# Kernel tuning notes

Measured on AMD Instinct MI355X. Metric: run time of the kernel, lower is better.

Reference implementation:

```python
import jax, jax.numpy as jnp
import numpy as np

B, S, D, H, DH = 2, 2048, 768, 12, 64
ROT, BASE, WIN = 64, 10000.0, 128
SCALE = float(np.sqrt(DH))  # cfg.attn_scale = sqrt(d_head) = 8.0


def _sin_cos():
    # TransformerLens calculate_sin_cos_rotary, rotary_adjacent_pairs=False
    pos = jnp.arange(S, dtype=jnp.float32)
    freq = BASE ** (jnp.arange(0, ROT, 2, dtype=jnp.float32) / ROT)
    freq = jnp.concatenate([freq, freq])  # 'd -> (2 d)'
    angles = pos[:, None] / freq[None, :]  # [S, ROT]
    return jnp.sin(angles), jnp.cos(angles)


def _rotate_every_two(v):
    n = v.shape[-1] // 2
    return jnp.concatenate([-v[..., n:], v[..., :n]], axis=-1)


def _apply_rotary(x, sin, cos):
    # x: [B, S, H, DH]; rotate first ROT dims, pass rest through
    xr, xp = x[..., :ROT], x[..., ROT:]
    c = cos[None, :, None, :]
    s = sin[None, :, None, :]
    return jnp.concatenate([xr * c + _rotate_every_two(xr) * s, xp], axis=-1)


def setup_inputs() -> dict:
    key = jax.random.key(0)
    ks = jax.random.split(key, 7)
    init = lambda k, shape: jax.random.normal(k, shape, jnp.float32) / np.sqrt(D).astype(np.float32)
    return dict(
        query_input=jax.random.normal(ks[0], (B, S, D), jnp.float32),
        key_input=jax.random.normal(ks[1], (B, S, D), jnp.float32),
        value_input=jax.random.normal(ks[2], (B, S, D), jnp.float32),
        W_Q=init(ks[3], (H, D, DH)),
        W_K=init(ks[4], (H, D, DH)),
        W_V=init(ks[5], (H, D, DH)),
        W_O=init(ks[6], (H, DH, D)),
        b_Q=jnp.zeros((H, DH), jnp.float32),
        b_K=jnp.zeros((H, DH), jnp.float32),
        b_V=jnp.zeros((H, DH), jnp.float32),
        b_O=jnp.zeros((D,), jnp.float32),
    )


def reference(query_input, key_input, value_input, W_Q, W_K, W_V, W_O, b_Q, b_K, b_V, b_O):
    # QKV projections (calculate_qkv_matrices)
    q = jnp.einsum('bpd,hdk->bphk', query_input, W_Q) + b_Q
    k = jnp.einsum('bpd,hdk->bphk', key_input, W_K) + b_K
    v = jnp.einsum('bpd,hdk->bphk', value_input, W_V) + b_V
    # rotary (kv_cache_pos_offset = 0)
    sin, cos = _sin_cos()
    q = _apply_rotary(q, sin, cos)
    k = _apply_rotary(k, sin, cos)
    # attention scores
    scores = jnp.einsum('bqhd,bkhd->bhqk', q, k) / SCALE
    # position_bias defaults to zeros -> no-op
    i = jnp.arange(S)[:, None]
    j = jnp.arange(S)[None, :]
    mask = (j <= i) & (j > i - WIN)
    scores = jnp.where(mask[None, None], scores, -jnp.inf)
    pattern = jax.nn.softmax(scores, axis=-1)
    pattern = jnp.where(jnp.isnan(pattern), 0.0, pattern)
    z = jnp.einsum('bhqk,bkhd->bqhd', pattern, v)  # [B, S, H, DH]
    # output projection: z flattened @ W_O (rearranged) + b_O
    out = z.reshape(B, S, H * DH) @ W_O.reshape(H * DH, D) + b_O
    return out
```

## Files before the change

kernel.cpp:

```cpp
#include <hip/hip_runtime.h>
#include <hip/hip_bf16.h>

#define BB 2
#define SS 2048
#define DD 768
#define HH 12
#define DHH 64
#define WIN 128
#define MM (BB*SS)

typedef __attribute__((ext_vector_type(8))) short bfrag;
typedef __attribute__((ext_vector_type(4))) float f32x4;
typedef __attribute__((ext_vector_type(4))) short s16x4;

#define AS3(p) ((__attribute__((address_space(3))) void*)(p))
#define AS1(p) ((const __attribute__((address_space(1))) void*)(p))

__device__ inline unsigned short f2bf(float f) {
    union { __hip_bfloat16 h; unsigned short u; } cv;
    cv.h = __float2bfloat16(f);
    return cv.u;
}

__global__ __launch_bounds__(256) void pack_kernel(
    const float* __restrict__ Xq, const float* __restrict__ Xk, const float* __restrict__ Xv,
    const float* __restrict__ Wq, const float* __restrict__ Wk, const float* __restrict__ Wv,
    const float* __restrict__ Wo,
    unsigned short* __restrict__ Wt, unsigned short* __restrict__ Wot,
    float2* __restrict__ rope, unsigned short* __restrict__ Xbf)
{
    __shared__ float T[64][65];
    const int bid = blockIdx.x, t = threadIdx.x;
    if (bid < 432) {
        int proj = bid / 144, rem = bid % 144;
        int h = rem / 12, d0 = (rem % 12) * 64;
        const float* src = (proj == 0 ? Wq : (proj == 1 ? Wk : Wv)) + (size_t)h * DD * DHH;
        int row = t >> 2, c0 = (t & 3) * 16;
        const float4* p4 = reinterpret_cast<const float4*>(src + (size_t)(d0 + row) * DHH + c0);
        float4 x0 = p4[0], x1 = p4[1], x2 = p4[2], x3 = p4[3];
        float* tr = &T[row][c0];
        tr[0]=x0.x; tr[1]=x0.y; tr[2]=x0.z; tr[3]=x0.w;
        tr[4]=x1.x; tr[5]=x1.y; tr[6]=x1.z; tr[7]=x1.w;
        tr[8]=x2.x; tr[9]=x2.y; tr[10]=x2.z; tr[11]=x2.w;
        tr[12]=x3.x; tr[13]=x3.y; tr[14]=x3.z; tr[15]=x3.w;
        __syncthreads();
        int dh = t >> 2;
        unsigned short tmp[16];
        #pragma unroll
        for (int j = 0; j < 16; j++) tmp[j] = f2bf(T[c0 + j][dh]);
        unsigned short* dst = Wt + (size_t)proj * DD * DD + (size_t)(h * 64 + dh) * DD + d0 + c0;
        *reinterpret_cast<bfrag*>(dst)     = *reinterpret_cast<bfrag*>(tmp);
        *reinterpret_cast<bfrag*>(dst + 8) = *reinterpret_cast<bfrag*>(tmp + 8);
    } else if (bid < 576) {
        int id2 = bid - 432;
        int k0 = (id2 / 12) * 64, n0 = (id2 % 12) * 64;
        int row = t >> 2, c0 = (t & 3) * 16;
        const float4* p4 = reinterpret_cast<const float4*>(Wo + (size_t)(k0 + row) * DD + n0 + c0);
        float4 x0 = p4[0], x1 = p4[1], x2 = p4[2], x3 = p4[3];
        float* tr = &T[row][c0];
        tr[0]=x0.x; tr[1]=x0.y; tr[2]=x0.z; tr[3]=x0.w;
        tr[4]=x1.x; tr[5]=x1.y; tr[6]=x1.z; tr[7]=x1.w;
        tr[8]=x2.x; tr[9]=x2.y; tr[10]=x2.z; tr[11]=x2.w;
        tr[12]=x3.x; tr[13]=x3.y; tr[14]=x3.z; tr[15]=x3.w;
        __syncthreads();
        int nr = t >> 2;
        unsigned short tmp[16];
        #pragma unroll
        for (int j = 0; j < 16; j++) tmp[j] = f2bf(T[c0 + j][nr]);
        unsigned short* dst = Wot + (size_t)(n0 + nr) * DD + k0 + c0;
        *reinterpret_cast<bfrag*>(dst)     = *reinterpret_cast<bfrag*>(tmp);
        *reinterpret_cast<bfrag*>(dst + 8) = *reinterpret_cast<bfrag*>(tmp + 8);
    } else if (bid < 832) {
        int idx = (bid - 576) * 256 + t;
        int p = idx >> 5, i2 = idx & 31;
        float inv_freq = exp2f(-(float)i2 * (13.287712379549449f / 32.0f));
        float s, c;
        sincosf((float)p * inv_freq, &s, &c);
        rope[idx] = make_float2(s, c);
    } else {
        int i = bid - 832;
        int proj = i / 768;
        size_t off = (size_t)(i % 768) * 4096 + t * 16;
        const float* src = (proj == 0 ? Xq : (proj == 1 ? Xk : Xv)) + off;
        const float4* p4 = reinterpret_cast<const float4*>(src);
        float4 a0 = p4[0], a1 = p4[1], a2 = p4[2], a3 = p4[3];
        unsigned short u[16];
        u[0]=f2bf(a0.x); u[1]=f2bf(a0.y); u[2]=f2bf(a0.z); u[3]=f2bf(a0.w);
        u[4]=f2bf(a1.x); u[5]=f2bf(a1.y); u[6]=f2bf(a1.z); u[7]=f2bf(a1.w);
        u[8]=f2bf(a2.x); u[9]=f2bf(a2.y); u[10]=f2bf(a2.z); u[11]=f2bf(a2.w);
        u[12]=f2bf(a3.x); u[13]=f2bf(a3.y); u[14]=f2bf(a3.z); u[15]=f2bf(a3.w);
        unsigned short* dst = Xbf + (size_t)proj * MM * DD + off;
        *reinterpret_cast<bfrag*>(dst)     = *reinterpret_cast<bfrag*>(u);
        *reinterpret_cast<bfrag*>(dst + 8) = *reinterpret_cast<bfrag*>(u + 8);
    }
}

__global__ __launch_bounds__(256) void qkv_gemm_kernel(
    const unsigned short* __restrict__ Xbf,
    const unsigned short* __restrict__ Wt,
    const float* __restrict__ bq, const float* __restrict__ bk, const float* __restrict__ bv,
    const float2* __restrict__ rope,
    unsigned short* __restrict__ qo, unsigned short* __restrict__ ko, unsigned short* __restrict__ vo)
{
    const int mt0  = blockIdx.x * 64;
    const int n0   = blockIdx.y * 128;
    const int proj = blockIdx.z;
    const unsigned short* X = Xbf + (size_t)proj * MM * DD + (size_t)mt0 * DD;
    const unsigned short* W = Wt + (size_t)proj * DD * DD + (size_t)n0 * DD;
    const float* bias = proj == 0 ? bq : (proj == 1 ? bk : bv);

    __shared__ unsigned short smem[12288];

    const int t = threadIdx.x;
    const int l = t & 63, w4 = t >> 6;
    const int l16 = l & 15, quad = l >> 4;
    const int wr = w4 >> 1, wc = w4 & 1;
    const int swz = (l16 >> 1) & 3;

    f32x4 acc[8] = {};

    #define STAGE_QKV(bufp, k0)                                                   \
        _Pragma("unroll")                                                         \
        for (int j = 0; j < 3; j++) {                                             \
            int g = w4 * 3 + j;                                                   \
            if (g < 4) {                                                          \
                int e = g * 512 + l * 8;                                          \
                int row = e >> 5;                                                 \
                int k8 = ((e >> 3) & 3) ^ ((row >> 1) & 3);                       \
                __builtin_amdgcn_global_load_lds(                                 \
                    AS1(X + (size_t)row * DD + (k0) + k8 * 8),                    \
                    AS3((bufp) + g * 512), 16, 0, 0);                             \
            } else {                                                              \
                int g2 = g - 4;                                                   \
                int e = g2 * 512 + l * 8;                                         \
                int row = e >> 5;                                                 \
                int k8 = ((e >> 3) & 3) ^ ((row >> 1) & 3);                       \
                __builtin_amdgcn_global_load_lds(                                 \
                    AS1(W + (size_t)row * DD + (k0) + k8 * 8),                    \
                    AS3((bufp) + 2048 + g2 * 512), 16, 0, 0);                     \
            }                                                                     \
        }

    STAGE_QKV(smem, 0)

    for (int it = 0; it < 24; ++it) {
        unsigned short* cur = smem + (it & 1) * 6144;
        __syncthreads();
        if (it < 23) {
            unsigned short* nxt = smem + ((it + 1) & 1) * 6144;
            STAGE_QKV(nxt, (it + 1) * 32)
        }
        bfrag af[2], bg[4];
        #pragma unroll
        for (int mi = 0; mi < 2; mi++)
            af[mi] = *reinterpret_cast<const bfrag*>(&cur[(wr * 32 + mi * 16 + l16) * 32 + ((quad ^ swz) * 8)]);
        #pragma unroll
        for (int ni = 0; ni < 4; ni++)
            bg[ni] = *reinterpret_cast<const bfrag*>(&cur[2048 + (wc * 64 + ni * 16 + l16) * 32 + ((quad ^ swz) * 8)]);
        #pragma unroll
        for (int mi = 0; mi < 2; mi++)
            #pragma unroll
            for (int ni = 0; ni < 4; ni++)
                acc[mi * 4 + ni] = __builtin_amdgcn_mfma_f32_16x16x32_bf16(af[mi], bg[ni], acc[mi * 4 + ni], 0, 0, 0);
    }
    __syncthreads();

    unsigned short* Ct = smem;
    const int b = mt0 >> 11;
    const int p0 = mt0 & (SS - 1);
    if (proj < 2) {
        #pragma unroll
        for (int ni = 0; ni < 4; ni++) {
            int nloc = wc * 64 + ni * 16 + l16;
            int n = n0 + nloc;
            int dh = n & 63;
            float bv0 = bias[n];
            float bv1 = bias[n ^ 32];
            float sgn = (dh & 32) ? 1.0f : -1.0f;
            const float2* rp = rope + (dh & 31);
            #pragma unroll
            for (int mi = 0; mi < 2; mi++)
                #pragma unroll
                for (int r = 0; r < 4; r++) {
                    int ploc = wr * 32 + mi * 16 + quad * 4 + r;
                    float2 sc = rp[(p0 + ploc) << 5];
                    float val = acc[mi * 4 + ni][r] + bv0;
                    float pr  = acc[mi * 4 + (ni ^ 2)][r] + bv1;
                    Ct[ploc * 140 + nloc] = f2bf(val * sc.y + sgn * pr * sc.x);
                }
        }
        __syncthreads();
        unsigned short* dst = (proj == 0) ? qo : ko;
        #pragma unroll
        for (int jj = 0; jj < 4; jj++) {
            int id = jj * 256 + t;
            int row = id >> 4, c = (id & 15) * 8;
            int n = n0 + c, h = n >> 6, dh = n & 63;
            bfrag vv = *reinterpret_cast<const bfrag*>(&Ct[row * 140 + c]);
            *reinterpret_cast<bfrag*>(dst + (((size_t)(b * HH + h) * SS + p0 + row) << 6) + dh) = vv;
        }
    } else {
        #pragma unroll
        for (int ni = 0; ni < 4; ni++) {
            int nloc = wc * 64 + ni * 16 + l16;
            float bv0 = bias[n0 + nloc];
            #pragma unroll
            for (int mi = 0; mi < 2; mi++)
                #pragma unroll
                for (int r = 0; r < 4; r++) {
                    int ploc = wr * 32 + mi * 16 + quad * 4 + r;
                    Ct[nloc * 72 + ploc] = f2bf(acc[mi * 4 + ni][r] + bv0);
                }
        }
        __syncthreads();
        #pragma unroll
        for (int jj = 0; jj < 4; jj++) {
            int id = jj * 256 + t;
            int row = id >> 3, c = (id & 7) * 8;
            int n = n0 + row, h = n >> 6, dh = n & 63;
            bfrag vv = *reinterpret_cast<const bfrag*>(&Ct[row * 72 + c]);
            *reinterpret_cast<bfrag*>(vo + (((size_t)(b * HH + h) * DHH + dh) << 11) + p0 + c) = vv;
        }
    }
    #undef STAGE_QKV
}

__global__ __launch_bounds__(256) void attn_kernel(
    const unsigned short* __restrict__ q,
    const unsigned short* __restrict__ k,
    const unsigned short* __restrict__ v,
    unsigned short* __restrict__ z)
{
    const int qb = blockIdx.x * 64;
    const int h  = blockIdx.y;
    const int b  = blockIdx.z;
    const int kb = qb - WIN;

    __shared__ unsigned short sA[12800];

    const int t = threadIdx.x;
    const int w4 = t >> 6, l = t & 63;
    const int l16 = l & 15, quad = l >> 4;
    const int swz = (l16 >> 1) & 3;

    const size_t qkbase = (size_t)(b * HH + h) * SS * DHH;
    const unsigned short* kp = (k + qkbase) + (ptrdiff_t)kb * DHH;
    const unsigned short* vp = (v + (size_t)(b * HH + h) * DHH * SS) + (ptrdiff_t)kb;

    #pragma unroll
    for (int j = 0; j < 6; j++) {
        int g = w4 * 6 + j;
        int panel = g >> 2, sub = g & 3;
        int rg = panel >> 1, kpart = panel & 1;
        int e = sub * 512 + l * 8;
        int row = e >> 5;
        int k8 = ((e >> 3) & 3) ^ ((row >> 1) & 3);
        __builtin_amdgcn_global_load_lds(
            AS1(kp + (size_t)(rg * 64 + row) * DHH + kpart * 32 + k8 * 8),
            AS3(sA + panel * 2048 + sub * 512), 16, 0, 0);
    }
    bfrag qf[2];
    #pragma unroll
    for (int kk = 0; kk < 2; kk++)
        qf[kk] = *reinterpret_cast<const bfrag*>(
            q + qkbase + (size_t)(qb + 16 * w4 + l16) * DHH + kk * 32 + quad * 8);
    bfrag vfA[12];
    #pragma unroll
    for (int ci = 0; ci < 3; ci++)
        #pragma unroll
        for (int mt = 0; mt < 4; mt++)
            vfA[ci * 4 + mt] = *reinterpret_cast<const bfrag*>(
                vp + (size_t)(16 * mt + l16) * SS + ci * 32 + quad * 8);

    __syncthreads();

    f32x4 sacc[12] = {};
    #pragma unroll
    for (int kk = 0; kk < 2; kk++)
        #pragma unroll
        for (int mt = 0; mt < 12; mt++) {
            int kr = 16 * mt + l16;
            bfrag bf = *reinterpret_cast<const bfrag*>(
                &sA[(((kr >> 6) * 2 + kk) * 2048) + (kr & 63) * 32 + ((quad ^ swz) * 8)]);
            sacc[mt] = __builtin_amdgcn_mfma_f32_16x16x32_bf16(qf[kk], bf, sacc[mt], 0, 0, 0);
        }

    bfrag vfB[12];
    #pragma unroll
    for (int ci = 0; ci < 3; ci++)
        #pragma unroll
        for (int mt = 0; mt < 4; mt++)
            vfB[ci * 4 + mt] = *reinterpret_cast<const bfrag*>(
                vp + (size_t)(16 * mt + l16) * SS + (ci + 3) * 32 + quad * 8);

    float mx[4] = {-3e38f, -3e38f, -3e38f, -3e38f};
    #pragma unroll
    for (int mt = 0; mt < 12; mt++)
        #pragma unroll
        for (int r = 0; r < 4; r++) {
            int row = 16 * w4 + quad * 4 + r;
            int c = 16 * mt + l16;
            bool valid = (c > row) && (c <= row + WIN) && (kb + c >= 0);
            float s = valid ? sacc[mt][r] * 0.125f : -3e38f;
            sacc[mt][r] = s;
            mx[r] = fmaxf(mx[r], s);
        }
    #pragma unroll
    for (int off = 1; off < 16; off <<= 1)
        #pragma unroll
        for (int r = 0; r < 4; r++) mx[r] = fmaxf(mx[r], __shfl_xor(mx[r], off, 64));
    float sum[4] = {0.f, 0.f, 0.f, 0.f};
    #pragma unroll
    for (int mt = 0; mt < 12; mt++)
        #pragma unroll
        for (int r = 0; r < 4; r++) {
            float p = __expf(sacc[mt][r] - mx[r]);
            sacc[mt][r] = p;
            sum[r] += p;
        }
    #pragma unroll
    for (int off = 1; off < 16; off <<= 1)
        #pragma unroll
        for (int r = 0; r < 4; r++) sum[r] += __shfl_xor(sum[r], off, 64);
    float inv[4];
    #pragma unroll
    for (int r = 0; r < 4; r++) inv[r] = 1.0f / sum[r];

    __syncthreads();

    unsigned short* Ps = sA;
    #pragma unroll
    for (int mt = 0; mt < 12; mt++)
        #pragma unroll
        for (int r = 0; r < 4; r++)
            Ps[(16 * w4 + quad * 4 + r) * 200 + 16 * mt + l16] = f2bf(sacc[mt][r] * inv[r]);

    f32x4 zacc[4] = {};
    #pragma unroll
    for (int ci = 0; ci < 6; ci++) {
        bfrag pb = *reinterpret_cast<const bfrag*>(
            &Ps[(16 * w4 + l16) * 200 + ci * 32 + quad * 8]);
        #pragma unroll
        for (int mt = 0; mt < 4; mt++) {
            bfrag va = (ci < 3) ? vfA[ci * 4 + mt] : vfB[(ci - 3) * 4 + mt];
            zacc[mt] = __builtin_amdgcn_mfma_f32_16x16x32_bf16(va, pb, zacc[mt], 0, 0, 0);
        }
    }
    size_t zrow = ((size_t)(b * SS + qb + 16 * w4 + l16)) * (HH * DHH) + h * DHH;
    #pragma unroll
    for (int mt = 0; mt < 4; mt++) {
        s16x4 pk;
        pk[0] = (short)f2bf(zacc[mt][0]);
        pk[1] = (short)f2bf(zacc[mt][1]);
        pk[2] = (short)f2bf(zacc[mt][2]);
        pk[3] = (short)f2bf(zacc[mt][3]);
        *reinterpret_cast<s16x4*>(z + zrow + 16 * mt + quad * 4) = pk;
    }
}

__device__ inline void stage128(unsigned short* dst, const unsigned short* src,
                                int w4, int l) {
    #pragma unroll
    for (int j = 0; j < 2; j++) {
        int eoff = (w4 * 2 + j) * 512;
        int e = eoff + l * 8;
        int row = e >> 5;
        int k8 = ((e >> 3) & 3) ^ ((row >> 1) & 3);
        __builtin_amdgcn_global_load_lds(AS1(src + (size_t)row * DD + k8 * 8),
                                         AS3(dst + eoff), 16, 0, 0);
    }
}
__device__ inline void stage64(unsigned short* dst, const unsigned short* src,
                               int w4, int l) {
    int eoff = w4 * 512;
    int e = eoff + l * 8;
    int row = e >> 5;
    int k8 = ((e >> 3) & 3) ^ ((row >> 1) & 3);
    __builtin_amdgcn_global_load_lds(AS1(src + (size_t)row * DD + k8 * 8),
                                     AS3(dst + eoff), 16, 0, 0);
}

__global__ __launch_bounds__(256) void out_gemm_kernel(
    const unsigned short* __restrict__ Z,
    const unsigned short* __restrict__ Wot,
    const float* __restrict__ bo,
    float* __restrict__ out)
{
    const int mt0 = blockIdx.x * 64;
    const int n0  = blockIdx.y * 128;
    const unsigned short* A = Z + (size_t)mt0 * DD;
    const unsigned short* Bw = Wot + (size_t)n0 * DD;

    __shared__ unsigned short smem[12288];

    const int t = threadIdx.x;
    const int l = t & 63, w4 = t >> 6;
    const int l16 = l & 15, quad = l >> 4;
    const int swz = (l16 >> 1) & 3;

    f32x4 acc[8] = {};

    stage64 (smem,        A,  w4, l);
    stage128(smem + 2048, Bw, w4, l);

    for (int it = 0; it < 24; ++it) {
        unsigned short* Ac = smem + (it & 1) * 6144;
        unsigned short* Bc = Ac + 2048;
        __syncthreads();
        if (it < 23) {
            unsigned short* An = smem + ((it + 1) & 1) * 6144;
            stage64 (An,        A  + (it + 1) * 32, w4, l);
            stage128(An + 2048, Bw + (it + 1) * 32, w4, l);
        }
        bfrag af[4], bg[2];
        #pragma unroll
        for (int mi = 0; mi < 4; mi++)
            af[mi] = *reinterpret_cast<const bfrag*>(&Ac[(mi * 16 + l16) * 32 + ((quad ^ swz) * 8)]);
        #pragma unroll
        for (int ni = 0; ni < 2; ni++)
            bg[ni] = *reinterpret_cast<const bfrag*>(&Bc[(w4 * 32 + ni * 16 + l16) * 32 + ((quad ^ swz) * 8)]);
        #pragma unroll
        for (int mi = 0; mi < 4; mi++)
            #pragma unroll
            for (int ni = 0; ni < 2; ni++)
                acc[mi * 2 + ni] = __builtin_amdgcn_mfma_f32_16x16x32_bf16(af[mi], bg[ni], acc[mi * 2 + ni], 0, 0, 0);
    }

    #pragma unroll
    for (int ni = 0; ni < 2; ni++) {
        int n = n0 + w4 * 32 + ni * 16 + l16;
        float bv0 = bo[n];
        #pragma unroll
        for (int mi = 0; mi < 4; mi++)
            #pragma unroll
            for (int r = 0; r < 4; r++) {
                int m = mt0 + mi * 16 + quad * 4 + r;
                out[(size_t)m * DD + n] = acc[mi * 2 + ni][r] + bv0;
            }
    }
}

extern "C" void kernel_launch(void* const* d_in, const int* in_sizes, int n_in,
                              void* d_out, int out_size, void* d_ws, size_t ws_size,
                              hipStream_t stream) {
    const float* Xq = (const float*)d_in[0];
    const float* Xk = (const float*)d_in[1];
    const float* Xv = (const float*)d_in[2];
    const float* Wq = (const float*)d_in[3];
    const float* Wk = (const float*)d_in[4];
    const float* Wv = (const float*)d_in[5];
    const float* Wo = (const float*)d_in[6];
    const float* bq = (const float*)d_in[7];
    const float* bk = (const float*)d_in[8];
    const float* bv = (const float*)d_in[9];
    const float* bo = (const float*)d_in[10];
    float* out = (float*)d_out;

    const size_t seg = (size_t)BB * HH * SS * DHH;
    unsigned short* q   = (unsigned short*)d_ws;
    unsigned short* k   = q + seg;
    unsigned short* v   = k + seg;
    unsigned short* z   = v + seg;
    unsigned short* Wt  = z + seg;
    unsigned short* Wot = Wt + (size_t)3 * DD * DD;
    float2* rope = (float2*)(Wot + (size_t)DD * DD);
    unsigned short* Xbf = (unsigned short*)(rope + 2048 * 32);

    pack_kernel<<<dim3(3136), 256, 0, stream>>>(Xq, Xk, Xv, Wq, Wk, Wv, Wo, Wt, Wot, rope, Xbf);
    qkv_gemm_kernel<<<dim3(MM / 64, DD / 128, 3), 256, 0, stream>>>(
        Xbf, Wt, bq, bk, bv, rope, q, k, v);
    attn_kernel<<<dim3(SS / 64, HH, BB), 256, 0, stream>>>(q, k, v, z);
    out_gemm_kernel<<<dim3(MM / 64, DD / 128), 256, 0, stream>>>(z, Wot, bo, out);
}
```

Baseline: 169.0 us.

## Enlarge QKV GEMM tile to 128x128 and stage V through LDS in attention

Measured after the change: 164.4 us. -2.7%, faster.

```diff
diff --git a/kernel.cpp b/kernel.cpp
--- a/kernel.cpp
+++ b/kernel.cpp
@@ -20,6 +20,28 @@
     union { __hip_bfloat16 h; unsigned short u; } cv;
     cv.h = __float2bfloat16(f);
     return cv.u;
+}
+
+__device__ inline void stage128(unsigned short* dst, const unsigned short* src,
+                                int w4, int l) {
+    #pragma unroll
+    for (int j = 0; j < 2; j++) {
+        int eoff = (w4 * 2 + j) * 512;
+        int e = eoff + l * 8;
+        int row = e >> 5;
+        int k8 = ((e >> 3) & 3) ^ ((row >> 1) & 3);
+        __builtin_amdgcn_global_load_lds(AS1(src + (size_t)row * DD + k8 * 8),
+                                         AS3(dst + eoff), 16, 0, 0);
+    }
+}
+__device__ inline void stage64(unsigned short* dst, const unsigned short* src,
+                               int w4, int l) {
+    int eoff = w4 * 512;
+    int e = eoff + l * 8;
+    int row = e >> 5;
+    int k8 = ((e >> 3) & 3) ^ ((row >> 1) & 3);
+    __builtin_amdgcn_global_load_lds(AS1(src + (size_t)row * DD + k8 * 8),
+                                     AS3(dst + eoff), 16, 0, 0);
 }
 
 __global__ __launch_bounds__(256) void pack_kernel(
@@ -102,14 +124,14 @@
     const float2* __restrict__ rope,
     unsigned short* __restrict__ qo, unsigned short* __restrict__ ko, unsigned short* __restrict__ vo)
 {
-    const int mt0  = blockIdx.x * 64;
+    const int mt0  = blockIdx.x * 128;
     const int n0   = blockIdx.y * 128;
     const int proj = blockIdx.z;
     const unsigned short* X = Xbf + (size_t)proj * MM * DD + (size_t)mt0 * DD;
     const unsigned short* W = Wt + (size_t)proj * DD * DD + (size_t)n0 * DD;
     const float* bias = proj == 0 ? bq : (proj == 1 ? bk : bv);
 
-    __shared__ unsigned short smem[12288];
+    __shared__ unsigned short smem[128 * 140];
 
     const int t = threadIdx.x;
     const int l = t & 63, w4 = t >> 6;
@@ -117,48 +139,29 @@
     const int wr = w4 >> 1, wc = w4 & 1;
     const int swz = (l16 >> 1) & 3;
 
-    f32x4 acc[8] = {};
-
-    #define STAGE_QKV(bufp, k0)                                                   \
-        _Pragma("unroll")                                                         \
-        for (int j = 0; j < 3; j++) {                                             \
-            int g = w4 * 3 + j;                                                   \
-            if (g < 4) {                                                          \
-                int e = g * 512 + l * 8;                                          \
-                int row = e >> 5;                                                 \
-                int k8 = ((e >> 3) & 3) ^ ((row >> 1) & 3);                       \
-                __builtin_amdgcn_global_load_lds(                                 \
-                    AS1(X + (size_t)row * DD + (k0) + k8 * 8),                    \
-                    AS3((bufp) + g * 512), 16, 0, 0);                             \
-            } else {                                                              \
-                int g2 = g - 4;                                                   \
-                int e = g2 * 512 + l * 8;                                         \
-                int row = e >> 5;                                                 \
-                int k8 = ((e >> 3) & 3) ^ ((row >> 1) & 3);                       \
-                __builtin_amdgcn_global_load_lds(                                 \
-                    AS1(W + (size_t)row * DD + (k0) + k8 * 8),                    \
-                    AS3((bufp) + 2048 + g2 * 512), 16, 0, 0);                     \
-            }                                                                     \
-        }
-
-    STAGE_QKV(smem, 0)
+    f32x4 acc[16] = {};
+
+    stage128(smem,        X, w4, l);
+    stage128(smem + 4096, W, w4, l);
 
     for (int it = 0; it < 24; ++it) {
-        unsigned short* cur = smem + (it & 1) * 6144;
+        unsigned short* Ac = smem + (it & 1) * 8192;
+        unsigned short* Bc = Ac + 4096;
         __syncthreads();
         if (it < 23) {
-            unsigned short* nxt = smem + ((it + 1) & 1) * 6144;
-            STAGE_QKV(nxt, (it + 1) * 32)
-        }
-        bfrag af[2], bg[4];
-        #pragma unroll
-        for (int mi = 0; mi < 2; mi++)
-            af[mi] = *reinterpret_cast<const bfrag*>(&cur[(wr * 32 + mi * 16 + l16) * 32 + ((quad ^ swz) * 8)]);
+            unsigned short* An = smem + ((it + 1) & 1) * 8192;
+            stage128(An,        X + (it + 1) * 32, w4, l);
+            stage128(An + 4096, W + (it + 1) * 32, w4, l);
+        }
+        bfrag af[4], bg[4];
+        #pragma unroll
+        for (int mi = 0; mi < 4; mi++)
+            af[mi] = *reinterpret_cast<const bfrag*>(&Ac[(wr * 64 + mi * 16 + l16) * 32 + ((quad ^ swz) * 8)]);
         #pragma unroll
         for (int ni = 0; ni < 4; ni++)
-            bg[ni] = *reinterpret_cast<const bfrag*>(&cur[2048 + (wc * 64 + ni * 16 + l16) * 32 + ((quad ^ swz) * 8)]);
-        #pragma unroll
-        for (int mi = 0; mi < 2; mi++)
+            bg[ni] = *reinterpret_cast<const bfrag*>(&Bc[(wc * 64 + ni * 16 + l16) * 32 + ((quad ^ swz) * 8)]);
+        #pragma unroll
+        for (int mi = 0; mi < 4; mi++)
             #pragma unroll
             for (int ni = 0; ni < 4; ni++)
                 acc[mi * 4 + ni] = __builtin_amdgcn_mfma_f32_16x16x32_bf16(af[mi], bg[ni], acc[mi * 4 + ni], 0, 0, 0);
@@ -167,7 +170,6 @@
 
     unsigned short* Ct = smem;
     const int b = mt0 >> 11;
-    const int p0 = mt0 & (SS - 1);
     if (proj < 2) {
         #pragma unroll
         for (int ni = 0; ni < 4; ni++) {
@@ -179,11 +181,12 @@
             float sgn = (dh & 32) ? 1.0f : -1.0f;
             const float2* rp = rope + (dh & 31);
             #pragma unroll
-            for (int mi = 0; mi < 2; mi++)
+            for (int mi = 0; mi < 4; mi++)
                 #pragma unroll
                 for (int r = 0; r < 4; r++) {
-                    int ploc = wr * 32 + mi * 16 + quad * 4 + r;
-                    float2 sc = rp[(p0 + ploc) << 5];
+                    int ploc = wr * 64 + mi * 16 + quad * 4 + r;
+                    int p = (mt0 + ploc) & (SS - 1);
+                    float2 sc = rp[p << 5];
                     float val = acc[mi * 4 + ni][r] + bv0;
                     float pr  = acc[mi * 4 + (ni ^ 2)][r] + bv1;
                     Ct[ploc * 140 + nloc] = f2bf(val * sc.y + sgn * pr * sc.x);
@@ -192,12 +195,13 @@
         __syncthreads();
         unsigned short* dst = (proj == 0) ? qo : ko;
         #pragma unroll
-        for (int jj = 0; jj < 4; jj++) {
+        for (int jj = 0; jj < 8; jj++) {
             int id = jj * 256 + t;
             int row = id >> 4, c = (id & 15) * 8;
             int n = n0 + c, h = n >> 6, dh = n & 63;
+            int p = (mt0 + row) & (SS - 1);
             bfrag vv = *reinterpret_cast<const bfrag*>(&Ct[row * 140 + c]);
-            *reinterpret_cast<bfrag*>(dst + (((size_t)(b * HH + h) * SS + p0 + row) << 6) + dh) = vv;
+            *reinterpret_cast<bfrag*>(dst + (((size_t)(b * HH + h) * SS + p) << 6) + dh) = vv;
         }
     } else {
         #pragma unroll
@@ -205,24 +209,24 @@
             int nloc = wc * 64 + ni * 16 + l16;
             float bv0 = bias[n0 + nloc];
             #pragma unroll
-            for (int mi = 0; mi < 2; mi++)
+            for (int mi = 0; mi < 4; mi++)
                 #pragma unroll
                 for (int r = 0; r < 4; r++) {
-                    int ploc = wr * 32 + mi * 16 + quad * 4 + r;
-                    Ct[nloc * 72 + ploc] = f2bf(acc[mi * 4 + ni][r] + bv0);
+                    int ploc = wr * 64 + mi * 16 + quad * 4 + r;
+                    Ct[nloc * 140 + ploc] = f2bf(acc[mi * 4 + ni][r] + bv0);
                 }
         }
         __syncthreads();
-        #pragma unroll
-        for (int jj = 0; jj < 4; jj++) {
+        int p0 = mt0 & (SS - 1);
+        #pragma unroll
+        for (int jj = 0; jj < 8; jj++) {
             int id = jj * 256 + t;
-            int row = id >> 3, c = (id & 7) * 8;
+            int row = id >> 4, c = (id & 15) * 8;
             int n = n0 + row, h = n >> 6, dh = n & 63;
-            bfrag vv = *reinterpret_cast<const bfrag*>(&Ct[row * 72 + c]);
+            bfrag vv = *reinterpret_cast<const bfrag*>(&Ct[row * 140 + c]);
             *reinterpret_cast<bfrag*>(vo + (((size_t)(b * HH + h) * DHH + dh) << 11) + p0 + c) = vv;
         }
     }
-    #undef STAGE_QKV
 }
 
 __global__ __launch_bounds__(256) void attn_kernel(
@@ -236,7 +240,7 @@
     const int b  = blockIdx.z;
     const int kb = qb - WIN;
 
-    __shared__ unsigned short sA[12800];
+    __shared__ unsigned short sA[25088];
 
     const int t = threadIdx.x;
     const int w4 = t >> 6, l = t & 63;
@@ -259,18 +263,21 @@
             AS1(kp + (size_t)(rg * 64 + row) * DHH + kpart * 32 + k8 * 8),
             AS3(sA + panel * 2048 + sub * 512), 16, 0, 0);
     }
+    #pragma unroll
+    for (int j = 0; j < 6; j++) {
+        int g = w4 * 6 + j;
+        int F = g * 64 + l;
+        int d = F / 24, s = F % 24;
+        int cs = s ^ (d & 7);
+        __builtin_amdgcn_global_load_lds(
+            AS1(vp + (size_t)d * SS + cs * 8),
+            AS3(sA + 12800 + g * 512), 16, 0, 0);
+    }
     bfrag qf[2];
     #pragma unroll
     for (int kk = 0; kk < 2; kk++)
         qf[kk] = *reinterpret_cast<const bfrag*>(
             q + qkbase + (size_t)(qb + 16 * w4 + l16) * DHH + kk * 32 + quad * 8);
-    bfrag vfA[12];
-    #pragma unroll
-    for (int ci = 0; ci < 3; ci++)
-        #pragma unroll
-        for (int mt = 0; mt < 4; mt++)
-            vfA[ci * 4 + mt] = *reinterpret_cast<const bfrag*>(
-                vp + (size_t)(16 * mt + l16) * SS + ci * 32 + quad * 8);
 
     __syncthreads();
 
@@ -284,14 +291,6 @@
                 &sA[(((kr >> 6) * 2 + kk) * 2048) + (kr & 63) * 32 + ((quad ^ swz) * 8)]);
             sacc[mt] = __builtin_amdgcn_mfma_f32_16x16x32_bf16(qf[kk], bf, sacc[mt], 0, 0, 0);
         }
-
-    bfrag vfB[12];
-    #pragma unroll
-    for (int ci = 0; ci < 3; ci++)
-        #pragma unroll
-        for (int mt = 0; mt < 4; mt++)
-            vfB[ci * 4 + mt] = *reinterpret_cast<const bfrag*>(
-                vp + (size_t)(16 * mt + l16) * SS + (ci + 3) * 32 + quad * 8);
 
     float mx[4] = {-3e38f, -3e38f, -3e38f, -3e38f};
     #pragma unroll
@@ -335,6 +334,7 @@
         for (int r = 0; r < 4; r++)
             Ps[(16 * w4 + quad * 4 + r) * 200 + 16 * mt + l16] = f2bf(sacc[mt][r] * inv[r]);
 
+    unsigned short* Vt = sA + 12800;
     f32x4 zacc[4] = {};
     #pragma unroll
     for (int ci = 0; ci < 6; ci++) {
@@ -342,7 +342,9 @@
             &Ps[(16 * w4 + l16) * 200 + ci * 32 + quad * 8]);
         #pragma unroll
         for (int mt = 0; mt < 4; mt++) {
-            bfrag va = (ci < 3) ? vfA[ci * 4 + mt] : vfB[(ci - 3) * 4 + mt];
+            int d = 16 * mt + l16;
+            bfrag va = *reinterpret_cast<const bfrag*>(
+                &Vt[d * 192 + (((ci * 4 + quad) ^ (l16 & 7)) * 8)]);
             zacc[mt] = __builtin_amdgcn_mfma_f32_16x16x32_bf16(va, pb, zacc[mt], 0, 0, 0);
         }
     }
@@ -356,28 +358,6 @@
         pk[3] = (short)f2bf(zacc[mt][3]);
         *reinterpret_cast<s16x4*>(z + zrow + 16 * mt + quad * 4) = pk;
     }
-}
-
-__device__ inline void stage128(unsigned short* dst, const unsigned short* src,
-                                int w4, int l) {
-    #pragma unroll
-    for (int j = 0; j < 2; j++) {
-        int eoff = (w4 * 2 + j) * 512;
-        int e = eoff + l * 8;
-        int row = e >> 5;
-        int k8 = ((e >> 3) & 3) ^ ((row >> 1) & 3);
-        __builtin_amdgcn_global_load_lds(AS1(src + (size_t)row * DD + k8 * 8),
-                                         AS3(dst + eoff), 16, 0, 0);
-    }
-}
-__device__ inline void stage64(unsigned short* dst, const unsigned short* src,
-                               int w4, int l) {
-    int eoff = w4 * 512;
-    int e = eoff + l * 8;
-    int row = e >> 5;
-    int k8 = ((e >> 3) & 3) ^ ((row >> 1) & 3);
-    __builtin_amdgcn_global_load_lds(AS1(src + (size_t)row * DD + k8 * 8),
-                                     AS3(dst + eoff), 16, 0, 0);
 }
 
 __global__ __launch_bounds__(256) void out_gemm_kernel(
@@ -467,7 +447,7 @@
     unsigned short* Xbf = (unsigned short*)(rope + 2048 * 32);
 
     pack_kernel<<<dim3(3136), 256, 0, stream>>>(Xq, Xk, Xv, Wq, Wk, Wv, Wo, Wt, Wot, rope, Xbf);
-    qkv_gemm_kernel<<<dim3(MM / 64, DD / 128, 3), 256, 0, stream>>>(
+    qkv_gemm_kernel<<<dim3(MM / 128, DD / 128, 3), 256, 0, stream>>>(
         Xbf, Wt, bq, bk, bv, rope, q, k, v);
     attn_kernel<<<dim3(SS / 64, HH, BB), 256, 0, stream>>>(q, k, v, z);
     out_gemm_kernel<<<dim3(MM / 64, DD / 128), 256, 0, stream>>>(z, Wot, bo, out);
```

## Stage V tile through LDS in attention and shrink out-GEMM tile to 64x64

Applied to the files above, without the earlier changes.

New measurement: 164.1 us. 2.9% less time.

```diff
diff --git a/kernel.cpp b/kernel.cpp
--- a/kernel.cpp
+++ b/kernel.cpp
@@ -20,6 +20,16 @@
     union { __hip_bfloat16 h; unsigned short u; } cv;
     cv.h = __float2bfloat16(f);
     return cv.u;
+}
+
+__device__ inline void stage64(unsigned short* dst, const unsigned short* src,
+                               int w4, int l) {
+    int eoff = w4 * 512;
+    int e = eoff + l * 8;
+    int row = e >> 5;
+    int k8 = ((e >> 3) & 3) ^ ((row >> 1) & 3);
+    __builtin_amdgcn_global_load_lds(AS1(src + (size_t)row * DD + k8 * 8),
+                                     AS3(dst + eoff), 16, 0, 0);
 }
 
 __global__ __launch_bounds__(256) void pack_kernel(
@@ -164,6 +174,7 @@
                 acc[mi * 4 + ni] = __builtin_amdgcn_mfma_f32_16x16x32_bf16(af[mi], bg[ni], acc[mi * 4 + ni], 0, 0, 0);
     }
     __syncthreads();
+    #undef STAGE_QKV
 
     unsigned short* Ct = smem;
     const int b = mt0 >> 11;
@@ -222,7 +233,6 @@
             *reinterpret_cast<bfrag*>(vo + (((size_t)(b * HH + h) * DHH + dh) << 11) + p0 + c) = vv;
         }
     }
-    #undef STAGE_QKV
 }
 
 __global__ __launch_bounds__(256) void attn_kernel(
@@ -236,7 +246,7 @@
     const int b  = blockIdx.z;
     const int kb = qb - WIN;
 
-    __shared__ unsigned short sA[12800];
+    __shared__ unsigned short sA[25088];
 
     const int t = threadIdx.x;
     const int w4 = t >> 6, l = t & 63;
@@ -259,18 +269,21 @@
             AS1(kp + (size_t)(rg * 64 + row) * DHH + kpart * 32 + k8 * 8),
             AS3(sA + panel * 2048 + sub * 512), 16, 0, 0);
     }
+    #pragma unroll
+    for (int j = 0; j < 6; j++) {
+        int g = w4 * 6 + j;
+        int F = g * 64 + l;
+        int d = F / 24, s = F % 24;
+        int cs = s ^ (d & 7);
+        __builtin_amdgcn_global_load_lds(
+            AS1(vp + (size_t)d * SS + cs * 8),
+            AS3(sA + 12800 + g * 512), 16, 0, 0);
+    }
     bfrag qf[2];
     #pragma unroll
     for (int kk = 0; kk < 2; kk++)
         qf[kk] = *reinterpret_cast<const bfrag*>(
             q + qkbase + (size_t)(qb + 16 * w4 + l16) * DHH + kk * 32 + quad * 8);
-    bfrag vfA[12];
-    #pragma unroll
-    for (int ci = 0; ci < 3; ci++)
-        #pragma unroll
-        for (int mt = 0; mt < 4; mt++)
-            vfA[ci * 4 + mt] = *reinterpret_cast<const bfrag*>(
-                vp + (size_t)(16 * mt + l16) * SS + ci * 32 + quad * 8);
 
     __syncthreads();
 
@@ -284,14 +297,6 @@
                 &sA[(((kr >> 6) * 2 + kk) * 2048) + (kr & 63) * 32 + ((quad ^ swz) * 8)]);
             sacc[mt] = __builtin_amdgcn_mfma_f32_16x16x32_bf16(qf[kk], bf, sacc[mt], 0, 0, 0);
         }
-
-    bfrag vfB[12];
-    #pragma unroll
-    for (int ci = 0; ci < 3; ci++)
-        #pragma unroll
-        for (int mt = 0; mt < 4; mt++)
-            vfB[ci * 4 + mt] = *reinterpret_cast<const bfrag*>(
-                vp + (size_t)(16 * mt + l16) * SS + (ci + 3) * 32 + quad * 8);
 
     float mx[4] = {-3e38f, -3e38f, -3e38f, -3e38f};
     #pragma unroll
@@ -335,6 +340,7 @@
         for (int r = 0; r < 4; r++)
             Ps[(16 * w4 + quad * 4 + r) * 200 + 16 * mt + l16] = f2bf(sacc[mt][r] * inv[r]);
 
+    unsigned short* Vt = sA + 12800;
     f32x4 zacc[4] = {};
     #pragma unroll
     for (int ci = 0; ci < 6; ci++) {
@@ -342,7 +348,9 @@
             &Ps[(16 * w4 + l16) * 200 + ci * 32 + quad * 8]);
         #pragma unroll
         for (int mt = 0; mt < 4; mt++) {
-            bfrag va = (ci < 3) ? vfA[ci * 4 + mt] : vfB[(ci - 3) * 4 + mt];
+            int d = 16 * mt + l16;
+            bfrag va = *reinterpret_cast<const bfrag*>(
+                &Vt[d * 192 + (((ci * 4 + quad) ^ (l16 & 7)) * 8)]);
             zacc[mt] = __builtin_amdgcn_mfma_f32_16x16x32_bf16(va, pb, zacc[mt], 0, 0, 0);
         }
     }
@@ -358,28 +366,6 @@
     }
 }
 
-__device__ inline void stage128(unsigned short* dst, const unsigned short* src,
-                                int w4, int l) {
-    #pragma unroll
-    for (int j = 0; j < 2; j++) {
-        int eoff = (w4 * 2 + j) * 512;
-        int e = eoff + l * 8;
-        int row = e >> 5;
-        int k8 = ((e >> 3) & 3) ^ ((row >> 1) & 3);
-        __builtin_amdgcn_global_load_lds(AS1(src + (size_t)row * DD + k8 * 8),
-                                         AS3(dst + eoff), 16, 0, 0);
-    }
-}
-__device__ inline void stage64(unsigned short* dst, const unsigned short* src,
-                               int w4, int l) {
-    int eoff = w4 * 512;
-    int e = eoff + l * 8;
-    int row = e >> 5;
-    int k8 = ((e >> 3) & 3) ^ ((row >> 1) & 3);
-    __builtin_amdgcn_global_load_lds(AS1(src + (size_t)row * DD + k8 * 8),
-                                     AS3(dst + eoff), 16, 0, 0);
-}
-
 __global__ __launch_bounds__(256) void out_gemm_kernel(
     const unsigned short* __restrict__ Z,
     const unsigned short* __restrict__ Wot,
@@ -387,56 +373,48 @@
     float* __restrict__ out)
 {
     const int mt0 = blockIdx.x * 64;
-    const int n0  = blockIdx.y * 128;
+    const int n0  = blockIdx.y * 64;
     const unsigned short* A = Z + (size_t)mt0 * DD;
     const unsigned short* Bw = Wot + (size_t)n0 * DD;
 
-    __shared__ unsigned short smem[12288];
+    __shared__ unsigned short smem[8192];
 
     const int t = threadIdx.x;
     const int l = t & 63, w4 = t >> 6;
     const int l16 = l & 15, quad = l >> 4;
     const int swz = (l16 >> 1) & 3;
 
-    f32x4 acc[8] = {};
-
-    stage64 (smem,        A,  w4, l);
-    stage128(smem + 2048, Bw, w4, l);
+    f32x4 acc[4] = {};
+
+    stage64(smem,        A,  w4, l);
+    stage64(smem + 2048, Bw, w4, l);
 
     for (int it = 0; it < 24; ++it) {
-        unsigned short* Ac = smem + (it & 1) * 6144;
+        unsigned short* Ac = smem + (it & 1) * 4096;
         unsigned short* Bc = Ac + 2048;
         __syncthreads();
         if (it < 23) {
-            unsigned short* An = smem + ((it + 1) & 1) * 6144;
-            stage64 (An,        A  + (it + 1) * 32, w4, l);
-            stage128(An + 2048, Bw + (it + 1) * 32, w4, l);
-        }
-        bfrag af[4], bg[2];
-        #pragma unroll
-        for (int mi = 0; mi < 4; mi++)
-            af[mi] = *reinterpret_cast<const bfrag*>(&Ac[(mi * 16 + l16) * 32 + ((quad ^ swz) * 8)]);
-        #pragma unroll
-        for (int ni = 0; ni < 2; ni++)
-            bg[ni] = *reinterpret_cast<const bfrag*>(&Bc[(w4 * 32 + ni * 16 + l16) * 32 + ((quad ^ swz) * 8)]);
-        #pragma unroll
-        for (int mi = 0; mi < 4; mi++)
-            #pragma unroll
-            for (int ni = 0; ni < 2; ni++)
-                acc[mi * 2 + ni] = __builtin_amdgcn_mfma_f32_16x16x32_bf16(af[mi], bg[ni], acc[mi * 2 + ni], 0, 0, 0);
-    }
-
-    #pragma unroll
-    for (int ni = 0; ni < 2; ni++) {
-        int n = n0 + w4 * 32 + ni * 16 + l16;
+            unsigned short* An = smem + ((it + 1) & 1) * 4096;
+            stage64(An,        A  + (it + 1) * 32, w4, l);
+            stage64(An + 2048, Bw + (it + 1) * 32, w4, l);
+        }
+        bfrag af = *reinterpret_cast<const bfrag*>(&Ac[(w4 * 16 + l16) * 32 + ((quad ^ swz) * 8)]);
+        #pragma unroll
+        for (int ni = 0; ni < 4; ni++) {
+            bfrag bg = *reinterpret_cast<const bfrag*>(&Bc[(ni * 16 + l16) * 32 + ((quad ^ swz) * 8)]);
+            acc[ni] = __builtin_amdgcn_mfma_f32_16x16x32_bf16(af, bg, acc[ni], 0, 0, 0);
+        }
+    }
+
+    #pragma unroll
+    for (int ni = 0; ni < 4; ni++) {
+        int n = n0 + ni * 16 + l16;
         float bv0 = bo[n];
         #pragma unroll
-        for (int mi = 0; mi < 4; mi++)
-            #pragma unroll
-            for (int r = 0; r < 4; r++) {
-                int m = mt0 + mi * 16 + quad * 4 + r;
-                out[(size_t)m * DD + n] = acc[mi * 2 + ni][r] + bv0;
-            }
+        for (int r = 0; r < 4; r++) {
+            int m = mt0 + w4 * 16 + quad * 4 + r;
+            out[(size_t)m * DD + n] = acc[ni][r] + bv0;
+        }
     }
 }
 
@@ -470,5 +448,5 @@
     qkv_gemm_kernel<<<dim3(MM / 64, DD / 128, 3), 256, 0, stream>>>(
         Xbf, Wt, bq, bk, bv, rope, q, k, v);
     attn_kernel<<<dim3(SS / 64, HH, BB), 256, 0, stream>>>(q, k, v, z);
-    out_gemm_kernel<<<dim3(MM / 64, DD / 128), 256, 0, stream>>>(z, Wot, bo, out);
-}
+    out_gemm_kernel<<<dim3(MM / 64, DD / 64), 256, 0, stream>>>(z, Wot, bo, out);
+}
```
